# Kernel tuning notes

Measured on AMD Instinct MI355X. Metric: run time of the kernel, lower is better.

The kernel has to match this reference:

```python
import jax, jax.numpy as jnp
import numpy as np

TEMPERATURE = 0.07


def setup_inputs() -> dict:
    key = jax.random.key(0)
    k1, k2 = jax.random.split(key)
    B, D = 4096, 512
    emb1 = jax.random.normal(k1, (B, D), dtype=jnp.float32)
    emb2 = jax.random.normal(k2, (B, D), dtype=jnp.float32)
    # module assumes L2-normalised embeddings
    emb1 = emb1 / jnp.linalg.norm(emb1, axis=-1, keepdims=True)
    emb2 = emb2 / jnp.linalg.norm(emb2, axis=-1, keepdims=True)
    return {"emb1": emb1, "emb2": emb2}


def reference(emb1, emb2):
    B = emb1.shape[0]
    emb = jnp.concatenate([emb1, emb2], axis=0)            # (2B, D)
    sim = jnp.einsum('id,jd->ij', emb, emb) / TEMPERATURE  # (2B, 2B)
    neg_inf = jnp.finfo(sim.dtype).min
    self_mask = jnp.eye(2 * B, dtype=bool)
    sim = jnp.where(self_mask, neg_inf, sim)
    labels = jnp.concatenate([jnp.arange(B, 2 * B), jnp.arange(B)])
    logp = jax.nn.log_softmax(sim, axis=-1)                # stable softmax CE
    nll = -jnp.take_along_axis(logp, labels[:, None], axis=-1)[:, 0]
    return jnp.mean(nll)
```

## Files before the change

### kernel.cpp

```cpp
#include <hip/hip_runtime.h>
#include <hip/hip_bf16.h>

#define B_    4096
#define D_    512
#define TB_   8192
#define BM    128
#define BK    128
#define NK    4
#define NTILE 64
#define NTRI  2080
#define INV_T 14.285714285714286f
#define SCL   (INV_T / 16129.0f)

typedef __attribute__((ext_vector_type(4))) int v4i;

#define GLOAD_LDS16(gp, lp)                                                        \
  __builtin_amdgcn_global_load_lds((const __attribute__((address_space(1))) void*)(gp), \
                                   (__attribute__((address_space(3))) void*)(lp),  \
                                   16, 0, 0)

__global__ void ntx_prep(const float* __restrict__ a, const float* __restrict__ b,
                         char* __restrict__ E8) {
  int t = blockIdx.x * blockDim.x + threadIdx.x;
  int i = t * 16;
  const float* src = (i < B_ * D_) ? (a + i) : (b + (i - B_ * D_));
  v4i o;
#pragma unroll
  for (int g = 0; g < 4; ++g) {
    float4 v = ((const float4*)src)[g];
    int q0 = __float2int_rn(v.x * 127.0f) & 255;
    int q1 = __float2int_rn(v.y * 127.0f) & 255;
    int q2 = __float2int_rn(v.z * 127.0f) & 255;
    int q3 = __float2int_rn(v.w * 127.0f) & 255;
    o[g] = q0 | (q1 << 8) | (q2 << 16) | (q3 << 24);
  }
  ((v4i*)E8)[t] = o;
}

__global__ __launch_bounds__(256, 4)
void ntx_sim(const char* __restrict__ E8, float* __restrict__ P,
             float* __restrict__ pos) {
  __shared__ __align__(16) char As[BM * BK];
  __shared__ __align__(16) char Bs[BM * BK];

  const int bid = blockIdx.x;
  const int t   = (bid & 7) * (NTRI / 8) + (bid >> 3);
  int ti = (int)((129.0f - sqrtf(16641.0f - 8.0f * (float)t)) * 0.5f);
  while (ti * (129 - ti) / 2 > t) --ti;
  while ((ti + 1) * (128 - ti) / 2 <= t) ++ti;
  const int tj = ti + (t - ti * (129 - ti) / 2);
  const int rowTile = ti * BM, colTile = tj * BM;
  const bool diag = (ti == tj);
  const bool posT = (tj == ti + B_ / BM);

  const int tid = threadIdx.x, lane = tid & 63, wave = tid >> 6;
  const int wr = wave >> 1, wc = wave & 1;
  const int llo = lane & 15, lhi = lane >> 4;

  const int srow = tid >> 3;
  const int ssc  = ((tid & 7) ^ (srow & 7)) << 4;
  const unsigned offA0  = (unsigned)(rowTile + srow) * D_ + ssc;
  const unsigned offB0  = (unsigned)(colTile + srow) * D_ + ssc;
  const unsigned ldsOf0 = (unsigned)tid * 16;

  const unsigned baseA = (unsigned)((wr * 64 + llo) * BK + ((lhi ^ (llo & 7)) << 4));
  const unsigned baseB = (unsigned)((wc * 64 + llo) * BK + ((lhi ^ (llo & 7)) << 4));

  v4i acc[4][4] = {};

  for (int kt = 0; kt < NK; ++kt) {
    const unsigned kb = (unsigned)kt * BK;
#pragma unroll
    for (int r = 0; r < 4; ++r) {
      GLOAD_LDS16(E8 + offA0 + r * 16384 + kb, &As[ldsOf0 + r * 4096]);
      GLOAD_LDS16(E8 + offB0 + r * 16384 + kb, &Bs[ldsOf0 + r * 4096]);
    }
    __syncthreads();
#pragma unroll
    for (int ks = 0; ks < 2; ++ks) {
      const unsigned bA = baseA ^ (ks * 64);
      const unsigned bB = baseB ^ (ks * 64);
      v4i af[4], bf[4];
#pragma unroll
      for (int m = 0; m < 4; ++m) {
        af[m] = *(const v4i*)&As[bA + m * 2048];
        bf[m] = *(const v4i*)&Bs[bB + m * 2048];
      }
#pragma unroll
      for (int m = 0; m < 4; ++m)
#pragma unroll
        for (int n = 0; n < 4; ++n)
          acc[m][n] = __builtin_amdgcn_mfma_i32_16x16x64_i8(af[m], bf[n],
                                                            acc[m][n], 0, 0, 0);
    }
    __syncthreads();
  }

  float* __restrict__ Prow = P + ((size_t)ti * 2 * NTILE + (size_t)tj * 2 + wc) * BM;
  float* __restrict__ Pcol = P + ((size_t)tj * 2 * NTILE + (size_t)ti * 2 + wr) * BM;
  float cs[4] = {0.f, 0.f, 0.f, 0.f};
#pragma unroll
  for (int m = 0; m < 4; ++m) {
    float rs[4] = {0.f, 0.f, 0.f, 0.f};
#pragma unroll
    for (int n = 0; n < 4; ++n) {
      int gc = colTile + wc * 64 + n * 16 + llo;
#pragma unroll
      for (int jj = 0; jj < 4; ++jj) {
        int gr = rowTile + wr * 64 + m * 16 + lhi * 4 + jj;
        float s = (float)acc[m][n][jj] * SCL;
        if (posT && gc - gr == B_) pos[gr] = s;
        float e = __expf(s);
        e = (diag && gr == gc) ? 0.0f : e;
        rs[jj] += e;
        cs[n]  += e;
      }
    }
#pragma unroll
    for (int jj = 0; jj < 4; ++jj) {
      float v = rs[jj];
      v += __shfl_xor(v, 1);
      v += __shfl_xor(v, 2);
      v += __shfl_xor(v, 4);
      v += __shfl_xor(v, 8);
      if (llo == 0) Prow[wr * 64 + m * 16 + lhi * 4 + jj] = v;
    }
  }
  if (!diag) {
#pragma unroll
    for (int n = 0; n < 4; ++n) {
      float v = cs[n];
      v += __shfl_xor(v, 16);
      v += __shfl_xor(v, 32);
      if (lhi == 0) Pcol[wc * 64 + n * 16 + llo] = v;
    }
  }
}

__global__ void ntx_fin1(const float* __restrict__ P, const float* __restrict__ pos,
                         float* __restrict__ par) {
  int r = blockIdx.x * 256 + threadIdx.x;
  int ti = r >> 7, rloc = r & 127;
  const float* base = P + (size_t)ti * 2 * NTILE * BM + rloc;
  float s = 0.f;
#pragma unroll 16
  for (int j = 0; j < 2 * NTILE; ++j) s += base[j * BM];
  float nll = __logf(s) - pos[r & (B_ - 1)];
  float v = nll;
#pragma unroll
  for (int off = 1; off < 64; off <<= 1) v += __shfl_xor(v, off);
  __shared__ float sm[4];
  if ((threadIdx.x & 63) == 0) sm[threadIdx.x >> 6] = v;
  __syncthreads();
  if (threadIdx.x == 0) par[blockIdx.x] = sm[0] + sm[1] + sm[2] + sm[3];
}

__global__ void ntx_fin2(const float* __restrict__ par, float* __restrict__ out) {
  int t = threadIdx.x;
  float s = (t < 32) ? par[t] : 0.f;
#pragma unroll
  for (int off = 1; off < 32; off <<= 1) s += __shfl_xor(s, off);
  if (t == 0) out[0] = s * (1.0f / TB_);
}

extern "C" void kernel_launch(void* const* d_in, const int* in_sizes, int n_in,
                              void* d_out, int out_size, void* d_ws, size_t ws_size,
                              hipStream_t stream) {
  const float* e1 = (const float*)d_in[0];
  const float* e2 = (const float*)d_in[1];
  float* out = (float*)d_out;
  char*  E8  = (char*)d_ws;
  float* P   = (float*)((char*)d_ws + (size_t)TB_ * D_);
  float* pos = P + (size_t)NTILE * 2 * NTILE * BM;
  float* par = pos + B_;

  ntx_prep<<<1024, 256, 0, stream>>>(e1, e2, E8);
  ntx_sim<<<NTRI, 256, 0, stream>>>(E8, P, pos);
  ntx_fin1<<<TB_ / 256, 256, 0, stream>>>(P, pos, par);
  ntx_fin2<<<1, 64, 0, stream>>>(par, out);
}
```

Before: 50.14 us.

## Pair adjacent triangle tiles per 512-thread block to share A-tile loads

Each block now handles two consecutive upper-triangle tiles with eight waves, four per tile. When both tiles share the same row tile, the A panel is loaded into LDS once and reused. The aim is to cut global-to-LDS traffic and halve the block count. In exchange LDS per block doubles to 64KB, which may lower occupancy, and launch_bounds(512,4) may squeeze registers.

```diff
diff --git a/kernel.cpp b/kernel.cpp
--- a/kernel.cpp
+++ b/kernel.cpp
@@ -9,6 +9,7 @@
 #define NK    4
 #define NTILE 64
 #define NTRI  2080
+#define NPAIR 1040
 #define INV_T 14.285714285714286f
 #define SCL   (INV_T / 16129.0f)
 
@@ -18,6 +19,14 @@
   __builtin_amdgcn_global_load_lds((const __attribute__((address_space(1))) void*)(gp), \
                                    (__attribute__((address_space(3))) void*)(lp),  \
                                    16, 0, 0)
+
+__device__ __forceinline__ void tri_decode(int u, int& ti, int& tj) {
+  int i = (int)((129.0f - sqrtf(16641.0f - 8.0f * (float)u)) * 0.5f);
+  while (i * (129 - i) / 2 > u) --i;
+  while ((i + 1) * (128 - i) / 2 <= u) ++i;
+  ti = i;
+  tj = i + (u - i * (129 - i) / 2);
+}
 
 __global__ void ntx_prep(const float* __restrict__ a, const float* __restrict__ b,
                          char* __restrict__ E8) {
@@ -37,43 +46,57 @@
   ((v4i*)E8)[t] = o;
 }
 
-__global__ __launch_bounds__(256, 4)
+__global__ __launch_bounds__(512, 4)
 void ntx_sim(const char* __restrict__ E8, float* __restrict__ P,
              float* __restrict__ pos) {
-  __shared__ __align__(16) char As[BM * BK];
-  __shared__ __align__(16) char Bs[BM * BK];
+  __shared__ __align__(16) char As[2][BM * BK];
+  __shared__ __align__(16) char Bs[2][BM * BK];
 
   const int bid = blockIdx.x;
-  const int t   = (bid & 7) * (NTRI / 8) + (bid >> 3);
-  int ti = (int)((129.0f - sqrtf(16641.0f - 8.0f * (float)t)) * 0.5f);
-  while (ti * (129 - ti) / 2 > t) --ti;
-  while ((ti + 1) * (128 - ti) / 2 <= t) ++ti;
-  const int tj = ti + (t - ti * (129 - ti) / 2);
+  const int pt  = (bid & 7) * (NPAIR / 8) + (bid >> 3);
+  int ti0, tj0, ti1, tj1;
+  tri_decode(2 * pt,     ti0, tj0);
+  tri_decode(2 * pt + 1, ti1, tj1);
+  const bool twoA = (ti1 != ti0);
+
+  const int tid = threadIdx.x, lane = tid & 63, wave = tid >> 6;
+  const int half = wave >> 2;
+  const int wr = (wave >> 1) & 1, wc = wave & 1;
+  const int llo = lane & 15, lhi = lane >> 4;
+
+  const int ti = half ? ti1 : ti0;
+  const int tj = half ? tj1 : tj0;
   const int rowTile = ti * BM, colTile = tj * BM;
   const bool diag = (ti == tj);
   const bool posT = (tj == ti + B_ / BM);
 
-  const int tid = threadIdx.x, lane = tid & 63, wave = tid >> 6;
-  const int wr = wave >> 1, wc = wave & 1;
-  const int llo = lane & 15, lhi = lane >> 4;
-
   const int srow = tid >> 3;
   const int ssc  = ((tid & 7) ^ (srow & 7)) << 4;
-  const unsigned offA0  = (unsigned)(rowTile + srow) * D_ + ssc;
-  const unsigned offB0  = (unsigned)(colTile + srow) * D_ + ssc;
+  const unsigned offA0  = (unsigned)(ti0 * BM + srow) * D_ + ssc;
+  const unsigned offA1  = (unsigned)(ti1 * BM + srow) * D_ + ssc;
+  const unsigned offB0  = (unsigned)(tj0 * BM + srow) * D_ + ssc;
+  const unsigned offB1  = (unsigned)(tj1 * BM + srow) * D_ + ssc;
   const unsigned ldsOf0 = (unsigned)tid * 16;
 
   const unsigned baseA = (unsigned)((wr * 64 + llo) * BK + ((lhi ^ (llo & 7)) << 4));
   const unsigned baseB = (unsigned)((wc * 64 + llo) * BK + ((lhi ^ (llo & 7)) << 4));
+  const char* Ab = &As[(half && twoA) ? 1 : 0][0];
+  const char* Bb = &Bs[half][0];
 
   v4i acc[4][4] = {};
 
   for (int kt = 0; kt < NK; ++kt) {
     const unsigned kb = (unsigned)kt * BK;
 #pragma unroll
-    for (int r = 0; r < 4; ++r) {
-      GLOAD_LDS16(E8 + offA0 + r * 16384 + kb, &As[ldsOf0 + r * 4096]);
-      GLOAD_LDS16(E8 + offB0 + r * 16384 + kb, &Bs[ldsOf0 + r * 4096]);
+    for (int r = 0; r < 2; ++r) {
+      GLOAD_LDS16(E8 + offA0 + r * 32768 + kb, &As[0][ldsOf0 + r * 8192]);
+      GLOAD_LDS16(E8 + offB0 + r * 32768 + kb, &Bs[0][ldsOf0 + r * 8192]);
+      GLOAD_LDS16(E8 + offB1 + r * 32768 + kb, &Bs[1][ldsOf0 + r * 8192]);
+    }
+    if (twoA) {
+#pragma unroll
+      for (int r = 0; r < 2; ++r)
+        GLOAD_LDS16(E8 + offA1 + r * 32768 + kb, &As[1][ldsOf0 + r * 8192]);
     }
     __syncthreads();
 #pragma unroll
@@ -83,8 +106,8 @@
       v4i af[4], bf[4];
 #pragma unroll
       for (int m = 0; m < 4; ++m) {
-        af[m] = *(const v4i*)&As[bA + m * 2048];
-        bf[m] = *(const v4i*)&Bs[bB + m * 2048];
+        af[m] = *(const v4i*)&Ab[bA + m * 2048];
+        bf[m] = *(const v4i*)&Bb[bB + m * 2048];
       }
 #pragma unroll
       for (int m = 0; m < 4; ++m)
@@ -175,7 +198,7 @@
   float* par = pos + B_;
 
   ntx_prep<<<1024, 256, 0, stream>>>(e1, e2, E8);
-  ntx_sim<<<NTRI, 256, 0, stream>>>(E8, P, pos);
+  ntx_sim<<<NPAIR, 512, 0, stream>>>(E8, P, pos);
   ntx_fin1<<<TB_ / 256, 256, 0, stream>>>(P, pos, par);
   ntx_fin2<<<1, 64, 0, stream>>>(par, out);
 }
```

Measured after the change: 56.98 us. 1.14x slower.

## Process four consecutive triangle tiles per block with prefetch across tiles

Applied to the files above, without the earlier changes.

The similarity kernel now launches a quarter as many blocks, each walking four consecutive upper-triangle tiles. The next k-slice, or the next tile's first slice, is loaded into LDS right after the MFMA work on the current slice, so the load can overlap the epilogue of the current tile. This trims block launch and index-decoding overhead. The cost is fewer blocks (520 for 256 CUs, with uneven per-CU counts), a lower occupancy hint, and a single LDS buffer, so loads still serialize with compute inside the k loop.

```diff
diff --git a/kernel.cpp b/kernel.cpp
--- a/kernel.cpp
+++ b/kernel.cpp
@@ -9,6 +9,7 @@
 #define NK    4
 #define NTILE 64
 #define NTRI  2080
+#define NPERS 520
 #define INV_T 14.285714285714286f
 #define SCL   (INV_T / 16129.0f)
 
@@ -37,21 +38,19 @@
   ((v4i*)E8)[t] = o;
 }
 
-__global__ __launch_bounds__(256, 4)
+__global__ __launch_bounds__(256, 2)
 void ntx_sim(const char* __restrict__ E8, float* __restrict__ P,
              float* __restrict__ pos) {
   __shared__ __align__(16) char As[BM * BK];
   __shared__ __align__(16) char Bs[BM * BK];
 
   const int bid = blockIdx.x;
-  const int t   = (bid & 7) * (NTRI / 8) + (bid >> 3);
-  int ti = (int)((129.0f - sqrtf(16641.0f - 8.0f * (float)t)) * 0.5f);
-  while (ti * (129 - ti) / 2 > t) --ti;
-  while ((ti + 1) * (128 - ti) / 2 <= t) ++ti;
-  const int tj = ti + (t - ti * (129 - ti) / 2);
-  const int rowTile = ti * BM, colTile = tj * BM;
-  const bool diag = (ti == tj);
-  const bool posT = (tj == ti + B_ / BM);
+  const int pb  = (bid & 7) * (NPERS / 8) + (bid >> 3);
+  const int t0  = pb * 4;
+  int ti = (int)((129.0f - sqrtf(16641.0f - 8.0f * (float)t0)) * 0.5f);
+  while (ti * (129 - ti) / 2 > t0) --ti;
+  while ((ti + 1) * (128 - ti) / 2 <= t0) ++ti;
+  int tj = ti + (t0 - ti * (129 - ti) / 2);
 
   const int tid = threadIdx.x, lane = tid & 63, wave = tid >> 6;
   const int wr = wave >> 1, wc = wave & 1;
@@ -59,81 +58,110 @@
 
   const int srow = tid >> 3;
   const int ssc  = ((tid & 7) ^ (srow & 7)) << 4;
-  const unsigned offA0  = (unsigned)(rowTile + srow) * D_ + ssc;
-  const unsigned offB0  = (unsigned)(colTile + srow) * D_ + ssc;
   const unsigned ldsOf0 = (unsigned)tid * 16;
-
   const unsigned baseA = (unsigned)((wr * 64 + llo) * BK + ((lhi ^ (llo & 7)) << 4));
   const unsigned baseB = (unsigned)((wc * 64 + llo) * BK + ((lhi ^ (llo & 7)) << 4));
 
-  v4i acc[4][4] = {};
-
-  for (int kt = 0; kt < NK; ++kt) {
-    const unsigned kb = (unsigned)kt * BK;
-#pragma unroll
-    for (int r = 0; r < 4; ++r) {
-      GLOAD_LDS16(E8 + offA0 + r * 16384 + kb, &As[ldsOf0 + r * 4096]);
-      GLOAD_LDS16(E8 + offB0 + r * 16384 + kb, &Bs[ldsOf0 + r * 4096]);
+  unsigned offA0 = (unsigned)(ti * BM + srow) * D_ + ssc;
+  unsigned offB0 = (unsigned)(tj * BM + srow) * D_ + ssc;
+
+#pragma unroll
+  for (int r = 0; r < 4; ++r) {
+    GLOAD_LDS16(E8 + offA0 + r * 16384, &As[ldsOf0 + r * 4096]);
+    GLOAD_LDS16(E8 + offB0 + r * 16384, &Bs[ldsOf0 + r * 4096]);
+  }
+
+  for (int it = 0; it < 4; ++it) {
+    const int rowTile = ti * BM, colTile = tj * BM;
+    const bool diag = (ti == tj);
+    const bool posT = (tj == ti + B_ / BM);
+    int nti = ti, ntj = tj + 1;
+    if (ntj == NTILE) { nti = ti + 1; ntj = nti; }
+    const unsigned offA0n = (unsigned)(nti * BM + srow) * D_ + ssc;
+    const unsigned offB0n = (unsigned)(ntj * BM + srow) * D_ + ssc;
+
+    v4i acc[4][4] = {};
+
+#pragma unroll
+    for (int kt = 0; kt < NK; ++kt) {
+      asm volatile("s_waitcnt vmcnt(0)" ::: "memory");
+      __builtin_amdgcn_s_barrier();
+#pragma unroll
+      for (int ks = 0; ks < 2; ++ks) {
+        const unsigned bA = baseA ^ (ks * 64);
+        const unsigned bB = baseB ^ (ks * 64);
+        v4i af[4], bf[4];
+#pragma unroll
+        for (int m = 0; m < 4; ++m) {
+          af[m] = *(const v4i*)&As[bA + m * 2048];
+          bf[m] = *(const v4i*)&Bs[bB + m * 2048];
+        }
+#pragma unroll
+        for (int m = 0; m < 4; ++m)
+#pragma unroll
+          for (int n = 0; n < 4; ++n)
+            acc[m][n] = __builtin_amdgcn_mfma_i32_16x16x64_i8(af[m], bf[n],
+                                                              acc[m][n], 0, 0, 0);
+      }
+      __builtin_amdgcn_s_barrier();
+      if (kt + 1 < NK) {
+        const unsigned kb = (unsigned)(kt + 1) * BK;
+#pragma unroll
+        for (int r = 0; r < 4; ++r) {
+          GLOAD_LDS16(E8 + offA0 + r * 16384 + kb, &As[ldsOf0 + r * 4096]);
+          GLOAD_LDS16(E8 + offB0 + r * 16384 + kb, &Bs[ldsOf0 + r * 4096]);
+        }
+      } else if (it + 1 < 4) {
+#pragma unroll
+        for (int r = 0; r < 4; ++r) {
+          GLOAD_LDS16(E8 + offA0n + r * 16384, &As[ldsOf0 + r * 4096]);
+          GLOAD_LDS16(E8 + offB0n + r * 16384, &Bs[ldsOf0 + r * 4096]);
+        }
+      }
     }
-    __syncthreads();
-#pragma unroll
-    for (int ks = 0; ks < 2; ++ks) {
-      const unsigned bA = baseA ^ (ks * 64);
-      const unsigned bB = baseB ^ (ks * 64);
-      v4i af[4], bf[4];
-#pragma unroll
-      for (int m = 0; m < 4; ++m) {
-        af[m] = *(const v4i*)&As[bA + m * 2048];
-        bf[m] = *(const v4i*)&Bs[bB + m * 2048];
-      }
-#pragma unroll
-      for (int m = 0; m < 4; ++m)
-#pragma unroll
-        for (int n = 0; n < 4; ++n)
-          acc[m][n] = __builtin_amdgcn_mfma_i32_16x16x64_i8(af[m], bf[n],
-                                                            acc[m][n], 0, 0, 0);
+
+    float* __restrict__ Prow = P + ((size_t)ti * 2 * NTILE + (size_t)tj * 2 + wc) * BM;
+    float* __restrict__ Pcol = P + ((size_t)tj * 2 * NTILE + (size_t)ti * 2 + wr) * BM;
+    float cs[4] = {0.f, 0.f, 0.f, 0.f};
+#pragma unroll
+    for (int m = 0; m < 4; ++m) {
+      float rs[4] = {0.f, 0.f, 0.f, 0.f};
+#pragma unroll
+      for (int n = 0; n < 4; ++n) {
+        int gc = colTile + wc * 64 + n * 16 + llo;
+#pragma unroll
+        for (int jj = 0; jj < 4; ++jj) {
+          int gr = rowTile + wr * 64 + m * 16 + lhi * 4 + jj;
+          float s = (float)acc[m][n][jj] * SCL;
+          if (posT && gc - gr == B_) pos[gr] = s;
+          float e = __expf(s);
+          e = (diag && gr == gc) ? 0.0f : e;
+          rs[jj] += e;
+          cs[n]  += e;
+        }
+      }
+#pragma unroll
+      for (int jj = 0; jj < 4; ++jj) {
+        float v = rs[jj];
+        v += __shfl_xor(v, 1);
+        v += __shfl_xor(v, 2);
+        v += __shfl_xor(v, 4);
+        v += __shfl_xor(v, 8);
+        if (llo == 0) Prow[wr * 64 + m * 16 + lhi * 4 + jj] = v;
+      }
     }
-    __syncthreads();
-  }
-
-  float* __restrict__ Prow = P + ((size_t)ti * 2 * NTILE + (size_t)tj * 2 + wc) * BM;
-  float* __restrict__ Pcol = P + ((size_t)tj * 2 * NTILE + (size_t)ti * 2 + wr) * BM;
-  float cs[4] = {0.f, 0.f, 0.f, 0.f};
-#pragma unroll
-  for (int m = 0; m < 4; ++m) {
-    float rs[4] = {0.f, 0.f, 0.f, 0.f};
-#pragma unroll
-    for (int n = 0; n < 4; ++n) {
-      int gc = colTile + wc * 64 + n * 16 + llo;
-#pragma unroll
-      for (int jj = 0; jj < 4; ++jj) {
-        int gr = rowTile + wr * 64 + m * 16 + lhi * 4 + jj;
-        float s = (float)acc[m][n][jj] * SCL;
-        if (posT && gc - gr == B_) pos[gr] = s;
-        float e = __expf(s);
-        e = (diag && gr == gc) ? 0.0f : e;
-        rs[jj] += e;
-        cs[n]  += e;
+    if (!diag) {
+#pragma unroll
+      for (int n = 0; n < 4; ++n) {
+        float v = cs[n];
+        v += __shfl_xor(v, 16);
+        v += __shfl_xor(v, 32);
+        if (lhi == 0) Pcol[wc * 64 + n * 16 + llo] = v;
       }
     }
-#pragma unroll
-    for (int jj = 0; jj < 4; ++jj) {
-      float v = rs[jj];
-      v += __shfl_xor(v, 1);
-      v += __shfl_xor(v, 2);
-      v += __shfl_xor(v, 4);
-      v += __shfl_xor(v, 8);
-      if (llo == 0) Prow[wr * 64 + m * 16 + lhi * 4 + jj] = v;
-    }
-  }
-  if (!diag) {
-#pragma unroll
-    for (int n = 0; n < 4; ++n) {
-      float v = cs[n];
-      v += __shfl_xor(v, 16);
-      v += __shfl_xor(v, 32);
-      if (lhi == 0) Pcol[wc * 64 + n * 16 + llo] = v;
-    }
+
+    ti = nti; tj = ntj;
+    offA0 = offA0n; offB0 = offB0n;
   }
 }
 
@@ -175,7 +203,7 @@
   float* par = pos + B_;
 
   ntx_prep<<<1024, 256, 0, stream>>>(e1, e2, E8);
-  ntx_sim<<<NTRI, 256, 0, stream>>>(E8, P, pos);
+  ntx_sim<<<NPERS, 256, 0, stream>>>(E8, P, pos);
   ntx_fin1<<<TB_ / 256, 256, 0, stream>>>(P, pos, par);
   ntx_fin2<<<1, 64, 0, stream>>>(par, out);
 }
```

Measured after the change: 57.95 us. 1.16x slower.
